# Kernel tuning notes

Hardware: AMD Instinct MI355X
Metric: run time of the kernel (lower is better)

The kernel has to match this reference:

```python
import jax, jax.numpy as jnp
import numpy as np

B, M, N, R, FD = 128, 64, 64, 8, 128
BN_EPS = 1e-5
GS_EPS = 1e-8


def conv2d(x, w, b):
    # x: [B,C,H,W], w: [O,C,3,3] or [O,C,1,1]
    y = jax.lax.conv_general_dilated(x, w, (1, 1), 'SAME',
                                     dimension_numbers=('NCHW', 'OIHW', 'NCHW'))
    return y + b[None, :, None, None]


def complex_conv(x, wr, br, wi, bi):
    cr = conv2d(x, wr, br)
    ci = conv2d(x, wi, bi)
    return jnp.concatenate([cr - ci, cr + ci], axis=1)


def batchnorm(x, g, b):
    # training-mode BN over (B,H,W)
    mean = x.mean(axis=(0, 2, 3), keepdims=True)
    var = ((x - mean) ** 2).mean(axis=(0, 2, 3), keepdims=True)
    return g[None, :, None, None] * (x - mean) * jax.lax.rsqrt(var + BN_EPS) + b[None, :, None, None]


def gram_schmidt(mat):
    # mat: [B, M, R, 2]; sequential over R (hard data dependency), vectorized over batch
    Rr = mat.shape[2]
    basis = []  # list of (vr, vi), each [B, M]
    for j in range(Rr):
        vr, vi = mat[:, :, j, 0], mat[:, :, j, 1]
        for br_, bi_ in basis:
            dot_real = jnp.sum(vr * br_ + vi * bi_, axis=1, keepdims=True)
            denom = jnp.sum(br_ * br_ + bi_ * bi_, axis=1, keepdims=True) + GS_EPS
            coef = dot_real / denom  # only real part used (as in torch code)
            vr = vr - coef * br_
            vi = vi - coef * bi_
        nrm = jnp.sqrt(jnp.sum(vr * vr + vi * vi, axis=1, keepdims=True) + GS_EPS)
        basis.append((vr / nrm, vi / nrm))
    return jnp.stack([jnp.stack(p, axis=-1) for p in basis], axis=2)  # [B,M,R,2]


def setup_inputs() -> dict:
    key = jax.random.key(0)
    ks = jax.random.split(key, 32)
    def p(i, shape, fan_in):
        return jax.random.normal(ks[i], shape, jnp.float32) / np.sqrt(fan_in)
    inp = {
        'x':   jax.random.normal(ks[0], (B, M, N, 2), jnp.float32),
        'w1r': p(1, (32, 2, 3, 3), 2 * 9),   'b1r': jnp.zeros((32,), jnp.float32),
        'w1i': p(2, (32, 2, 3, 3), 2 * 9),   'b1i': jnp.zeros((32,), jnp.float32),
        'g1':  jnp.ones((64,), jnp.float32), 'be1': jnp.zeros((64,), jnp.float32),
        'w2r': p(3, (64, 64, 3, 3), 64 * 9), 'b2r': jnp.zeros((64,), jnp.float32),
        'w2i': p(4, (64, 64, 3, 3), 64 * 9), 'b2i': jnp.zeros((64,), jnp.float32),
        'g2':  jnp.ones((128,), jnp.float32), 'be2': jnp.zeros((128,), jnp.float32),
        'w3r': p(5, (FD, 128, 3, 3), 128 * 9), 'b3r': jnp.zeros((FD,), jnp.float32),
        'w3i': p(6, (FD, 128, 3, 3), 128 * 9), 'b3i': jnp.zeros((FD,), jnp.float32),
        'g3':  jnp.ones((2 * FD,), jnp.float32), 'be3': jnp.zeros((2 * FD,), jnp.float32),
        'wu':  p(7, (2 * R, 2 * FD), 2 * FD), 'bu': jnp.zeros((2 * R,), jnp.float32),
        'ws':  p(8, (R, 2 * FD), 2 * FD),     'bs': jnp.zeros((R,), jnp.float32),
        'wv':  p(9, (2 * R, 2 * FD), 2 * FD), 'bv': jnp.zeros((2 * R,), jnp.float32),
    }
    return inp


def forward(x, w1r, b1r, w1i, b1i, g1, be1, w2r, b2r, w2i, b2i, g2, be2,
            w3r, b3r, w3i, b3i, g3, be3, wu, bu, ws, bs, wv, bv):
    h = jnp.transpose(x, (0, 3, 1, 2))  # [B,2,M,N]
    h = jax.nn.relu(batchnorm(complex_conv(h, w1r, b1r, w1i, b1i), g1, be1))
    h = jax.nn.relu(batchnorm(complex_conv(h, w2r, b2r, w2i, b2i), g2, be2))
    h = jax.nn.relu(batchnorm(complex_conv(h, w3r, b3r, w3i, b3i), g3, be3))  # [B,2FD,M,N]
    # u branch: avg over W, 1x1 conv (= channel matmul), relu
    pu = h.mean(axis=3)                                      # [B,2FD,M]
    u = jax.nn.relu(jnp.einsum('bcm,oc->bom', pu, wu) + bu[None, :, None])  # [B,2R,M]
    u = jnp.transpose(u, (0, 2, 1)).reshape(-1, M, R, 2)     # channel c = 2j+part
    u = gram_schmidt(u)
    # s branch: global avg pool + linear + relu
    ps = h.mean(axis=(2, 3))                                 # [B,2FD]
    s = jax.nn.relu(ps @ ws.T + bs)                          # [B,R]
    # v branch: avg over H, 1x1 conv, relu
    pv = h.mean(axis=2)                                      # [B,2FD,N]
    v = jax.nn.relu(jnp.einsum('bcn,oc->bon', pv, wv) + bv[None, :, None])  # [B,2R,N]
    v = jnp.transpose(v, (0, 2, 1)).reshape(-1, N, R, 2)
    v = gram_schmidt(v)
    return (u, s, v)


def reference(x, w1r, b1r, w1i, b1i, g1, be1, w2r, b2r, w2i, b2i, g2, be2,
              w3r, b3r, w3i, b3i, g3, be3, wu, bu, ws, bs, wv, bv):
    return forward(x, w1r, b1r, w1i, b1i, g1, be1, w2r, b2r, w2i, b2i, g2, be2,
                   w3r, b3r, w3i, b3i, g3, be3, wu, bu, ws, bs, wv, bv)
```

## Files before the change

### kernel.cpp

```cpp
#include <hip/hip_runtime.h>

typedef _Float16 f16;
typedef __attribute__((ext_vector_type(8))) short short8;
typedef __attribute__((ext_vector_type(8))) _Float16 half8;
typedef __attribute__((ext_vector_type(4))) float f32x4;

#define DEV __device__ __forceinline__

DEV float h2f(short s) { f16 h; __builtin_memcpy(&h, &s, 2); return (float)h; }
DEV short f2h(float f) { f16 h = (f16)f; short s; __builtin_memcpy(&s, &h, 2); return s; }
DEV half8 s2h8(short8 s) { half8 h; __builtin_memcpy(&h, &s, 16); return h; }

DEV float wave_sum(float v) {
    #pragma unroll
    for (int m = 1; m < 64; m <<= 1) v += __shfl_xor(v, m);
    return v;
}

__global__ __launch_bounds__(256) void prep_w_k(
    const float* __restrict__ wr, const float* __restrict__ wi,
    f16* __restrict__ wf, int CIN, int COUT)
{
    int idx = blockIdx.x * 256 + threadIdx.x;
    int KC = CIN >> 5, NG = (2 * COUT) >> 4;
    int total = 9 * KC * NG * 512;
    if (idx >= total) return;
    int j = idx & 7, lane = (idx >> 3) & 63;
    int t9 = idx >> 9;
    int gg = t9 % NG, s = t9 / NG;
    int kc = s % KC, tap = s / KC;
    int n = gg * 16 + (lane & 15);
    int cin = kc * 32 + (lane >> 4) * 8 + j;
    int o = n < COUT ? n : n - COUT;
    float sgn = n < COUT ? -1.f : 1.f;
    float wv = wr[(o * CIN + cin) * 9 + tap] + sgn * wi[(o * CIN + cin) * 9 + tap];
    wf[idx] = (f16)wv;
}

__global__ __launch_bounds__(256) void conv1_k(
    const float* __restrict__ x,
    const float* __restrict__ w1r, const float* __restrict__ w1i,
    f16* __restrict__ out)
{
    int idx = blockIdx.x * 256 + threadIdx.x;
    int b = idx >> 12, p = idx & 4095;
    int m = p >> 6, n = p & 63;

    float v[2][9];
    #pragma unroll
    for (int dy = 0; dy < 3; ++dy)
        #pragma unroll
        for (int dx = 0; dx < 3; ++dx) {
            int yy = m + dy - 1, xx = n + dx - 1;
            bool ok = (yy >= 0 && yy < 64 && xx >= 0 && xx < 64);
            int base = ((b * 64 + (ok ? yy : 0)) * 64 + (ok ? xx : 0)) * 2;
            v[0][dy*3+dx] = ok ? x[base]     : 0.f;
            v[1][dy*3+dx] = ok ? x[base + 1] : 0.f;
        }

    float o1[64];
    #pragma unroll
    for (int o = 0; o < 32; ++o) {
        float cr = 0.f, ci = 0.f;
        #pragma unroll
        for (int c = 0; c < 2; ++c)
            #pragma unroll
            for (int k = 0; k < 9; ++k) {
                cr = fmaf(v[c][k], w1r[(o*2+c)*9 + k], cr);
                ci = fmaf(v[c][k], w1i[(o*2+c)*9 + k], ci);
            }
        o1[o]      = cr - ci;
        o1[32 + o] = cr + ci;
    }
    f16* ob = out + (size_t)idx * 64;
    #pragma unroll
    for (int grp = 0; grp < 8; ++grp) {
        short8 pk;
        #pragma unroll
        for (int k = 0; k < 8; ++k) pk[k] = f2h(o1[grp*8 + k]);
        *(short8*)(ob + grp * 8) = pk;
    }
}

template<int C8>
__global__ __launch_bounds__(256) void statsv_k(
    const f16* __restrict__ t, float* __restrict__ stats, int iters)
{
    const int C = C8 * 8;
    __shared__ float ls[2 * C];
    const int tid = threadIdx.x;
    const int cg = tid & (C8 - 1), pg = tid / C8;
    const int NG = 256 / C8;
    for (int u = tid; u < 2 * C; u += 256) ls[u] = 0.f;
    __syncthreads();
    float s8[8] = {0,0,0,0,0,0,0,0}, q8[8] = {0,0,0,0,0,0,0,0};
    size_t base = (size_t)blockIdx.x * NG * iters + pg;
    for (int i = 0; i < iters; ++i) {
        size_t pp = base + (size_t)i * NG;
        short8 r = *(const short8*)(t + pp * C + cg * 8);
        #pragma unroll
        for (int k = 0; k < 8; ++k) { float v = h2f(r[k]); s8[k] += v; q8[k] += v * v; }
    }
    #pragma unroll
    for (int k = 0; k < 8; ++k) {
        atomicAdd(&ls[cg*8 + k], s8[k]);
        atomicAdd(&ls[C + cg*8 + k], q8[k]);
    }
    __syncthreads();
    for (int u = tid; u < C; u += 256) {
        atomicAdd(&stats[u], ls[u]);
        atomicAdd(&stats[C + u], ls[C + u]);
    }
}

__global__ void bnparam_k(const float* __restrict__ stats,
                          const float* __restrict__ g, const float* __restrict__ be,
                          float* __restrict__ sc, int C)
{
    int c = threadIdx.x;
    if (c >= C) return;
    const float invN = 1.f / (128.f * 4096.f);
    float mean  = stats[c] * invN;
    float var   = stats[C + c] * invN - mean * mean;
    float scale = g[c] * rsqrtf(var + 1e-5f);
    sc[c]     = scale;
    sc[C + c] = be[c] - mean * scale;
}

template<int CIN, bool CHUNK>
__global__ __launch_bounds__(256, 4) void conv_mfma_k(
    const f16* __restrict__ in, const f16* __restrict__ wf,
    const float* __restrict__ scin, f16* __restrict__ outp,
    float* __restrict__ stats, int n0, int NG, int statsC, int ostride)
{
    constexpr int KQ = CIN / 32;
    constexpr int NSTEP = KQ * 9;
    __shared__ char lds[4*64*72*2];
    __shared__ float lsts[4][64], lstq[4][64];
    char* actl = lds;
    const int flat = blockIdx.x;
    const int swzb = (flat & 7) * 256 + (flat >> 3);
    const int b = swzb >> 4, y0 = (swzb & 15) * 4;
    const int n0e = n0 + blockIdx.y * 64;
    const int tid = threadIdx.x, l = tid & 63, w = tid >> 6;
    const int li = l & 15, g = l >> 4;

    f32x4 acc[4][4];
    #pragma unroll
    for (int mf = 0; mf < 4; ++mf)
        #pragma unroll
        for (int nf = 0; nf < 4; ++nf)
            acc[mf][nf] = f32x4{0.f, 0.f, 0.f, 0.f};

    int swz[3];
    #pragma unroll
    for (int dx = 0; dx < 3; ++dx) swz[dx] = ((li + dx) & 7) << 4;

    const f16* wblk = wf + ((size_t)(n0e >> 4) << 9) + (l << 3);

    for (int st = 0; st < NSTEP; ++st) {
        const int kq = st / 9, tap = st - kq * 9;
        if (tap == 0) {
            half8 scl8, shf8;
            {
                int cb = kq*32 + (tid & 3) * 8;
                #pragma unroll
                for (int k = 0; k < 8; ++k) {
                    scl8[k] = (f16)scin[cb + k];
                    shf8[k] = (f16)scin[CIN + cb + k];
                }
            }
            __syncthreads();
            #pragma unroll
            for (int i = 0; i < 7; ++i) {
                int u = tid + i * 256;
                if (u < 6*66*4) {
                    int r = u / 264, rem = u - r * 264;
                    int sx = rem >> 2, cg = rem & 3;
                    int srow = y0 - 1 + r, gx = sx - 1;
                    short8 pk = {0,0,0,0,0,0,0,0};
                    if (srow >= 0 && srow < 64 && gx >= 0 && gx < 64) {
                        short8 raw = *(const short8*)(in +
                            ((size_t)(b*4096 + srow*64 + gx)) * CIN + kq*32 + cg*8);
                        half8 rv = s2h8(raw) * scl8 + shf8;
                        short8 sr; __builtin_memcpy(&sr, &rv, 16);
                        pk = sr & ~(sr >> 15);
                    }
                    int off = ((r*66 + sx)*32 + cg*8)*2 ^ ((sx & 7) << 4);
                    *(short8*)(actl + off) = pk;
                }
            }
            __syncthreads();
        }
        short8 breg[4];
        {
            int s = tap * KQ + kq;
            const f16* p = wblk + ((size_t)(s * NG) << 9);
            #pragma unroll
            for (int nf = 0; nf < 4; ++nf) breg[nf] = *(const short8*)(p + (nf << 9));
        }
        int dy = (tap * 11) >> 5, dx = tap - dy * 3;
        int r = w + dy;
        #pragma unroll
        for (int mf = 0; mf < 4; ++mf) {
            int sx = mf*16 + li + dx;
            half8 a = s2h8(*(const short8*)(actl + ((((r*66 + sx)*32) + g*8)*2 ^ swz[dx])));
            #pragma unroll
            for (int nf = 0; nf < 4; ++nf)
                acc[mf][nf] = __builtin_amdgcn_mfma_f32_16x16x32_f16(a, s2h8(breg[nf]), acc[mf][nf], 0, 0, 0);
        }
    }

    #pragma unroll
    for (int nf = 0; nf < 4; ++nf) {
        float s = 0.f, q = 0.f;
        #pragma unroll
        for (int mf = 0; mf < 4; ++mf)
            #pragma unroll
            for (int reg = 0; reg < 4; ++reg) {
                float v = acc[mf][nf][reg];
                s += v; q += v * v;
            }
        s += __shfl_xor(s, 16); s += __shfl_xor(s, 32);
        q += __shfl_xor(q, 16); q += __shfl_xor(q, 32);
        if (l < 16) { lsts[w][nf*16 + l] = s; lstq[w][nf*16 + l] = q; }
    }
    __syncthreads();
    if (tid < 64) {
        const int sb = CHUNK ? 0 : n0e;
        float s = lsts[0][tid] + lsts[1][tid] + lsts[2][tid] + lsts[3][tid];
        float q = lstq[0][tid] + lstq[1][tid] + lstq[2][tid] + lstq[3][tid];
        atomicAdd(&stats[sb + tid], s);
        atomicAdd(&stats[statsC + sb + tid], q);
    }

    f16* st = (f16*)lds;
    #pragma unroll
    for (int mf = 0; mf < 4; ++mf)
        #pragma unroll
        for (int nf = 0; nf < 4; ++nf)
            #pragma unroll
            for (int reg = 0; reg < 4; ++reg)
                st[(w*64 + mf*16 + g*4 + reg)*72 + nf*16 + li] = (f16)acc[mf][nf][reg];
    __syncthreads();
    const int obase = CHUNK ? 0 : n0e;
    const size_t pxbase = (size_t)b * 4096 + (size_t)y0 * 64;
    #pragma unroll
    for (int rd = 0; rd < 8; ++rd) {
        int u = rd * 256 + tid;
        int px = u >> 3, n8 = u & 7;
        short8 v = *(const short8*)(st + px*72 + n8*8);
        *(short8*)(outp + (pxbase + px) * ostride + obase + n8*8) = v;
    }
}

__global__ __launch_bounds__(256) void pool_k(
    const f16* __restrict__ t3c, const float* __restrict__ sc3c,
    float* __restrict__ pu, float* __restrict__ pv, int ncb)
{
    const int b = blockIdx.x, yh = blockIdx.y;
    const int t = threadIdx.x, cg = t & 7, xp = t >> 3;
    const int w = t >> 6, lane = t & 63;
    __shared__ float rq[4][16][64];
    float scl[8], shf[8];
    #pragma unroll
    for (int k = 0; k < 8; ++k) { scl[k] = sc3c[cg*8 + k]; shf[k] = sc3c[64 + cg*8 + k]; }
    float colacc[2][8];
    #pragma unroll
    for (int xi = 0; xi < 2; ++xi)
        #pragma unroll
        for (int k = 0; k < 8; ++k) colacc[xi][k] = 0.f;

    for (int yb = 0; yb < 2; ++yb) {
        for (int yy = 0; yy < 16; ++yy) {
            int y = yh*32 + yb*16 + yy;
            float rc[8];
            #pragma unroll
            for (int xi = 0; xi < 2; ++xi) {
                int xx = xp*2 + xi;
                short8 raw = *(const short8*)(t3c +
                    ((size_t)(b*4096 + y*64 + xx)) * 64 + cg*8);
                #pragma unroll
                for (int k = 0; k < 8; ++k) {
                    float v = fmaxf(fmaf(h2f(raw[k]), scl[k], shf[k]), 0.f);
                    colacc[xi][k] += v;
                    rc[k] = xi ? (rc[k] + v) : v;
                }
            }
            #pragma unroll
            for (int k = 0; k < 8; ++k) {
                rc[k] += __shfl_xor(rc[k], 8);
                rc[k] += __shfl_xor(rc[k], 16);
                rc[k] += __shfl_xor(rc[k], 32);
            }
            if (lane < 8) {
                #pragma unroll
                for (int k = 0; k < 8; ++k) rq[w][yy][lane*8 + k] = rc[k];
            }
        }
        __syncthreads();
        for (int u = t; u < 1024; u += 256) {
            int yy = u >> 6, c = u & 63;
            float v = rq[0][yy][c] + rq[1][yy][c] + rq[2][yy][c] + rq[3][yy][c];
            pu[((size_t)b*256 + ncb + c)*64 + (yh*32 + yb*16 + yy)] = v * (1.f/64.f);
        }
        __syncthreads();
    }
    #pragma unroll
    for (int xi = 0; xi < 2; ++xi)
        #pragma unroll
        for (int k = 0; k < 8; ++k)
            atomicAdd(&pv[((size_t)b*256 + ncb + cg*8 + k)*64 + xp*2 + xi],
                      colacc[xi][k] * (1.f/64.f));
}

__global__ __launch_bounds__(256) void headuv_k(
    const float* __restrict__ pool, const float* __restrict__ w,
    const float* __restrict__ bias, float* __restrict__ out)
{
    int b = blockIdx.x;
    int m = threadIdx.x & 63;
    int ob4 = threadIdx.x >> 6;
    float acc[4] = { bias[ob4], bias[ob4+4], bias[ob4+8], bias[ob4+12] };
    const float* pb = pool + (size_t)b * 256 * 64 + m;
    for (int c = 0; c < 256; ++c) {
        float v = pb[c * 64];
        #pragma unroll
        for (int i = 0; i < 4; ++i)
            acc[i] = fmaf(v, w[(ob4 + i*4) * 256 + c], acc[i]);
    }
    float* op = out + (size_t)b * 16 * 64 + m;
    #pragma unroll
    for (int i = 0; i < 4; ++i)
        op[(ob4 + i*4) * 64] = fmaxf(acc[i], 0.f);
}

__global__ __launch_bounds__(64) void heads_s_k(
    const float* __restrict__ pu, const float* __restrict__ wS,
    const float* __restrict__ bS, float* __restrict__ out)
{
    int b = blockIdx.x, lane = threadIdx.x;
    __shared__ float ls[256];
    for (int i = 0; i < 4; ++i) {
        const float* p = pu + ((size_t)b*256 + lane*4 + i) * 64;
        float s = 0.f;
        for (int m = 0; m < 64; ++m) s += p[m];
        ls[lane*4 + i] = s * (1.f/64.f);
    }
    __syncthreads();
    float acc[8] = {0,0,0,0,0,0,0,0};
    for (int c = lane; c < 256; c += 64) {
        float v = ls[c];
        #pragma unroll
        for (int o = 0; o < 8; ++o) acc[o] = fmaf(v, wS[o*256 + c], acc[o]);
    }
    #pragma unroll
    for (int o = 0; o < 8; ++o) acc[o] = wave_sum(acc[o]);
    if (lane == 0) {
        #pragma unroll
        for (int o = 0; o < 8; ++o)
            out[b*8 + o] = fmaxf(acc[o] + bS[o], 0.f);
    }
}

__global__ __launch_bounds__(64) void gs_k(
    const float* __restrict__ pre, float* __restrict__ out)
{
    int b = blockIdx.x, lane = threadIdx.x;
    const float* pb = pre + (size_t)b * 16 * 64 + lane;
    float vr[8], vi[8], den[8];
    #pragma unroll
    for (int j = 0; j < 8; ++j) { vr[j] = pb[(2*j)*64]; vi[j] = pb[(2*j+1)*64]; }

    #pragma unroll
    for (int j = 0; j < 8; ++j) {
        #pragma unroll
        for (int k = 0; k < j; ++k) {
            float d = wave_sum(vr[j]*vr[k] + vi[j]*vi[k]);
            float coef = d / den[k];
            vr[j] = fmaf(-coef, vr[k], vr[j]);
            vi[j] = fmaf(-coef, vi[k], vi[j]);
        }
        float n2 = wave_sum(vr[j]*vr[j] + vi[j]*vi[j]);
        float inv = 1.f / sqrtf(n2 + 1e-8f);
        vr[j] *= inv; vi[j] *= inv;
        float nn = wave_sum(vr[j]*vr[j] + vi[j]*vi[j]);
        den[j] = nn + 1e-8f;
    }
    float* ob = out + (size_t)b * 64 * 16 + lane * 16;
    #pragma unroll
    for (int j = 0; j < 8; ++j) { ob[j*2] = vr[j]; ob[j*2+1] = vi[j]; }
}

extern "C" void kernel_launch(void* const* d_in, const int* in_sizes, int n_in,
                              void* d_out, int out_size, void* d_ws, size_t ws_size,
                              hipStream_t stream)
{
    const float* x   = (const float*)d_in[0];
    const float* w1r = (const float*)d_in[1];
    const float* w1i = (const float*)d_in[3];
    const float* g1  = (const float*)d_in[5];
    const float* be1 = (const float*)d_in[6];
    const float* w2r = (const float*)d_in[7];
    const float* w2i = (const float*)d_in[9];
    const float* g2  = (const float*)d_in[11];
    const float* be2 = (const float*)d_in[12];
    const float* w3r = (const float*)d_in[13];
    const float* w3i = (const float*)d_in[15];
    const float* g3  = (const float*)d_in[17];
    const float* be3 = (const float*)d_in[18];
    const float* wu  = (const float*)d_in[19];
    const float* bu  = (const float*)d_in[20];
    const float* wS  = (const float*)d_in[21];
    const float* bS  = (const float*)d_in[22];
    const float* wv  = (const float*)d_in[23];
    const float* bv  = (const float*)d_in[24];
    float* out = (float*)d_out;

    char* ws = (char*)d_ws;
    f16*   t2     = (f16*)  (ws + 0);
    f16*   t1     = (f16*)  (ws + 134217728);
    f16*   t3c    = (f16*)  (ws + 134217728);
    float* upre   = (float*)(ws + 134217728);
    float* vpre   = (float*)(ws + 134742016);
    float* pu     = (float*)(ws + 201326592);
    float* pv     = (float*)(ws + 209715200);
    f16*   wfrag2 = (f16*)  (ws + 218103808);
    f16*   wfrag3 = (f16*)  (ws + 218103808);
    float* stats  = (float*)(ws + 219283456);
    float* scsh   = (float*)(ws + 219287040);
    float* stats1 = stats,  *stats2 = stats + 128;
    float* sc1    = scsh,   *sc2    = scsh  + 128, *sc3c = scsh + 384;

    hipMemsetAsync(stats, 0, 3584, stream);
    hipMemsetAsync(pv, 0, (size_t)128*256*64*4, stream);

    prep_w_k<<<288, 256, 0, stream>>>(w2r, w2i, wfrag2, 64, 64);

    conv1_k<<<2048, 256, 0, stream>>>(x, w1r, w1i, t1);
    statsv_k<8><<<1024, 256, 0, stream>>>(t1, stats1, 16);
    bnparam_k<<<1, 64, 0, stream>>>(stats1, g1, be1, sc1, 64);

    conv_mfma_k<64, false><<<dim3(2048, 2), 256, 0, stream>>>(
        t1, wfrag2, sc1, t2, stats2,
        0, 8, 128, 128);
    bnparam_k<<<1, 128, 0, stream>>>(stats2, g2, be2, sc2, 128);

    prep_w_k<<<1152, 256, 0, stream>>>(w3r, w3i, wfrag3, 128, 128);
    for (int nc = 0; nc < 4; ++nc) {
        conv_mfma_k<128, true><<<dim3(2048, 1), 256, 0, stream>>>(
            t2, wfrag3, sc2, t3c, stats + 384 + nc*128,
            nc*64, 16, 64, 64);
        bnparam_k<<<1, 64, 0, stream>>>(stats + 384 + nc*128, g3 + nc*64, be3 + nc*64, sc3c, 64);
        pool_k<<<dim3(128, 2), 256, 0, stream>>>(t3c, sc3c, pu, pv, nc*64);
    }

    headuv_k<<<128, 256, 0, stream>>>(pu, wu, bu, upre);
    headuv_k<<<128, 256, 0, stream>>>(pv, wv, bv, vpre);
    heads_s_k<<<128, 64, 0, stream>>>(pu, wS, bS, out + 131072);

    gs_k<<<128, 64, 0, stream>>>(upre, out);
    gs_k<<<128, 64, 0, stream>>>(vpre, out + 132096);
}
```

Baseline: 846.0 us.

## Stage conv weights per channel-chunk in LDS via direct global-to-LDS loads

```diff
diff --git a/kernel.cpp b/kernel.cpp
--- a/kernel.cpp
+++ b/kernel.cpp
@@ -28,7 +28,7 @@
     int j = idx & 7, lane = (idx >> 3) & 63;
     int t9 = idx >> 9;
     int gg = t9 % NG, s = t9 / NG;
-    int kc = s % KC, tap = s / KC;
+    int tap = s % 9, kc = s / 9;
     int n = gg * 16 + (lane & 15);
     int cin = kc * 32 + (lane >> 4) * 8 + j;
     int o = n < COUT ? n : n - COUT;
@@ -128,22 +128,22 @@
 }
 
 template<int CIN, bool CHUNK>
-__global__ __launch_bounds__(256, 4) void conv_mfma_k(
+__global__ __launch_bounds__(256, 2) void conv_mfma_k(
     const f16* __restrict__ in, const f16* __restrict__ wf,
     const float* __restrict__ scin, f16* __restrict__ outp,
     float* __restrict__ stats, int n0, int NG, int statsC, int ostride)
 {
     constexpr int KQ = CIN / 32;
-    constexpr int NSTEP = KQ * 9;
-    __shared__ char lds[4*64*72*2];
+    __shared__ char actl[6*66*32*2];
+    __shared__ char Bq[9*4*1024];
     __shared__ float lsts[4][64], lstq[4][64];
-    char* actl = lds;
     const int flat = blockIdx.x;
     const int swzb = (flat & 7) * 256 + (flat >> 3);
     const int b = swzb >> 4, y0 = (swzb & 15) * 4;
     const int n0e = n0 + blockIdx.y * 64;
     const int tid = threadIdx.x, l = tid & 63, w = tid >> 6;
     const int li = l & 15, g = l >> 4;
+    const int g0 = n0e >> 4;
 
     f32x4 acc[4][4];
     #pragma unroll
@@ -156,21 +156,24 @@
     #pragma unroll
     for (int dx = 0; dx < 3; ++dx) swz[dx] = ((li + dx) & 7) << 4;
 
-    const f16* wblk = wf + ((size_t)(n0e >> 4) << 9) + (l << 3);
-
-    for (int st = 0; st < NSTEP; ++st) {
-        const int kq = st / 9, tap = st - kq * 9;
-        if (tap == 0) {
+    for (int kq = 0; kq < KQ; ++kq) {
+        __syncthreads();
+        #pragma unroll
+        for (int j = 0; j < 9; ++j) {
+            const f16* src = wf + (((size_t)((kq*9 + j)*NG + g0 + w)) << 9) + (l << 3);
+            __builtin_amdgcn_global_load_lds(
+                (const __attribute__((address_space(1))) void*)src,
+                (__attribute__((address_space(3))) void*)&Bq[(j*4 + w)*1024],
+                16, 0, 0);
+        }
+        {
             half8 scl8, shf8;
-            {
-                int cb = kq*32 + (tid & 3) * 8;
-                #pragma unroll
-                for (int k = 0; k < 8; ++k) {
-                    scl8[k] = (f16)scin[cb + k];
-                    shf8[k] = (f16)scin[CIN + cb + k];
-                }
-            }
-            __syncthreads();
+            int cb = kq*32 + (tid & 3) * 8;
+            #pragma unroll
+            for (int k = 0; k < 8; ++k) {
+                scl8[k] = (f16)scin[cb + k];
+                shf8[k] = (f16)scin[CIN + cb + k];
+            }
             #pragma unroll
             for (int i = 0; i < 7; ++i) {
                 int u = tid + i * 256;
@@ -190,24 +193,24 @@
                     *(short8*)(actl + off) = pk;
                 }
             }
-            __syncthreads();
-        }
-        short8 breg[4];
-        {
-            int s = tap * KQ + kq;
-            const f16* p = wblk + ((size_t)(s * NG) << 9);
-            #pragma unroll
-            for (int nf = 0; nf < 4; ++nf) breg[nf] = *(const short8*)(p + (nf << 9));
-        }
-        int dy = (tap * 11) >> 5, dx = tap - dy * 3;
-        int r = w + dy;
-        #pragma unroll
-        for (int mf = 0; mf < 4; ++mf) {
-            int sx = mf*16 + li + dx;
-            half8 a = s2h8(*(const short8*)(actl + ((((r*66 + sx)*32) + g*8)*2 ^ swz[dx])));
+        }
+        __syncthreads();
+        #pragma unroll
+        for (int tap = 0; tap < 9; ++tap) {
+            half8 bb[4];
             #pragma unroll
             for (int nf = 0; nf < 4; ++nf)
-                acc[mf][nf] = __builtin_amdgcn_mfma_f32_16x16x32_f16(a, s2h8(breg[nf]), acc[mf][nf], 0, 0, 0);
+                bb[nf] = s2h8(*(const short8*)(Bq + (tap*4 + nf)*1024 + l*16));
+            int dy = (tap * 11) >> 5, dx = tap - dy * 3;
+            int r = w + dy;
+            #pragma unroll
+            for (int mf = 0; mf < 4; ++mf) {
+                int sx = mf*16 + li + dx;
+                half8 a = s2h8(*(const short8*)(actl + ((((r*66 + sx)*32) + g*8)*2 ^ swz[dx])));
+                #pragma unroll
+                for (int nf = 0; nf < 4; ++nf)
+                    acc[mf][nf] = __builtin_amdgcn_mfma_f32_16x16x32_f16(a, bb[nf], acc[mf][nf], 0, 0, 0);
+            }
         }
     }
 
@@ -234,7 +237,7 @@
         atomicAdd(&stats[statsC + sb + tid], q);
     }
 
-    f16* st = (f16*)lds;
+    f16* st = (f16*)Bq;
     #pragma unroll
     for (int mf = 0; mf < 4; ++mf)
         #pragma unroll
```

Result: no change. 849.3 us (+0.4%).
